# Kernel optimization log

Hardware: AMD Instinct MI355X
Metric: run time of the kernel (lower is better)

Reference implementation:

```python
import jax, jax.numpy as jnp
import numpy as np

Q_MAX = 127.0  # 2^(8-1) - 1 for 8-bit activations


def _ste_round(x):
    # forward: round(x); backward: identity
    return x + jax.lax.stop_gradient(jnp.round(x) - x)


def setup_inputs() -> dict:
    key = jax.random.key(0)
    k1, k2 = jax.random.split(key)
    B, S, D_IN, D_OUT = 4, 4096, 2048, 2048
    x = jax.random.normal(k1, (B, S, D_IN), dtype=jnp.float32)
    # muP-style init: std = 1/sqrt(fan_in)
    weight = jax.random.normal(k2, (D_OUT, D_IN), dtype=jnp.float32) / np.sqrt(D_IN)
    return {"x": x, "weight": weight}


def reference(x, weight):
    # --- ternary weight quantization (AbsMean) ---
    w_scale = jnp.maximum(jnp.mean(jnp.abs(weight)), 1e-6)        # scalar
    w_norm = weight / w_scale
    w_quant = jnp.clip(_ste_round(w_norm), -1.0, 1.0)             # [O, I], values in {-1,0,1}

    # --- per-token absmax activation quantization (8-bit) ---
    a_scale = jnp.clip(jnp.max(jnp.abs(x), axis=-1, keepdims=True), 1e-8, None)  # [B,S,1]
    x_quant = jnp.clip(_ste_round(x * (Q_MAX / a_scale)), -Q_MAX, Q_MAX)         # [B,S,I]

    # --- scaled matmul: y = (x_q @ w_q^T) * w_scale * (a_scale / Q_MAX) ---
    y = jnp.einsum('bsi,oi->bso', x_quant, w_quant)
    y = y * (w_scale * (a_scale / Q_MAX))
    return y
```

## Files before the change

### kernel.cpp

```cpp
#include <hip/hip_runtime.h>
#include <hip/hip_bf16.h>

typedef int int4v __attribute__((ext_vector_type(4)));

#define K_DIM 2048
#define N_DIM 2048
#define M_DIM 16384
#define NW 4194304
#define BKB 128
#define NKT (K_DIM / BKB)

__global__ void k_wsum(const float4* __restrict__ w4, double* __restrict__ red) {
  const int n4 = NW / 4;
  double s = 0.0;
  for (int i = blockIdx.x * blockDim.x + threadIdx.x; i < n4; i += gridDim.x * blockDim.x) {
    float4 v = w4[i];
    s += (double)fabsf(v.x) + (double)fabsf(v.y) + (double)fabsf(v.z) + (double)fabsf(v.w);
  }
  for (int o = 32; o; o >>= 1) s += __shfl_xor(s, o);
  __shared__ double sd[4];
  if ((threadIdx.x & 63) == 0) sd[threadIdx.x >> 6] = s;
  __syncthreads();
  if (threadIdx.x == 0) red[blockIdx.x] = (sd[0] + sd[1]) + (sd[2] + sd[3]);
}

__global__ void k_wscale(const double* __restrict__ red, double* __restrict__ wsd) {
  double s = red[threadIdx.x];
  for (int o = 32; o; o >>= 1) s += __shfl_xor(s, o);
  __shared__ double sd[4];
  if ((threadIdx.x & 63) == 0) sd[threadIdx.x >> 6] = s;
  __syncthreads();
  if (threadIdx.x == 0) {
    double m = ((sd[0] + sd[1]) + (sd[2] + sd[3])) / (double)NW;
    *wsd = (m > 1e-6) ? m : 1e-6;
  }
}

__device__ __forceinline__ char wq1(float v, double ws) {
  double r = rint((double)v / ws);
  r = fmin(fmax(r, -1.0), 1.0);
  return (char)(int)r;
}

__global__ void k_wquant(const float4* __restrict__ w4, const double* __restrict__ wsd,
                         char4* __restrict__ wq4) {
  int i = blockIdx.x * blockDim.x + threadIdx.x;
  if (i >= NW / 4) return;
  double ws = *wsd;
  float4 v = w4[i];
  char4 q;
  q.x = wq1(v.x, ws);
  q.y = wq1(v.y, ws);
  q.z = wq1(v.z, ws);
  q.w = wq1(v.w, ws);
  wq4[i] = q;
}

__device__ __forceinline__ char qi8(float v, double rr) {
  double q = rint((double)v * rr);
  q = fmin(fmax(q, -127.0), 127.0);
  return (char)(int)q;
}

__global__ void k_xquant(const float* __restrict__ x, float* __restrict__ ascale,
                         char* __restrict__ xq) {
  const int row = blockIdx.x;
  const int t = threadIdx.x;
  const float4* xr = (const float4*)(x + (size_t)row * K_DIM);
  float4 v0 = xr[t];
  float4 v1 = xr[t + 256];
  float m = fmaxf(fmaxf(fmaxf(fabsf(v0.x), fabsf(v0.y)), fmaxf(fabsf(v0.z), fabsf(v0.w))),
                  fmaxf(fmaxf(fabsf(v1.x), fabsf(v1.y)), fmaxf(fabsf(v1.z), fabsf(v1.w))));
  for (int o = 32; o; o >>= 1) m = fmaxf(m, __shfl_xor(m, o));
  __shared__ float sm[4];
  if ((t & 63) == 0) sm[t >> 6] = m;
  __syncthreads();
  float a = fmaxf(fmaxf(sm[0], sm[1]), fmaxf(sm[2], sm[3]));
  a = fmaxf(a, 1e-8f);
  if (t == 0) ascale[row] = a;
  double rr = 127.0 / (double)a;
  char4* qr4 = (char4*)(xq + (size_t)row * K_DIM);
  char4 a4, b4;
  a4.x = qi8(v0.x, rr); a4.y = qi8(v0.y, rr); a4.z = qi8(v0.z, rr); a4.w = qi8(v0.w, rr);
  b4.x = qi8(v1.x, rr); b4.y = qi8(v1.y, rr); b4.z = qi8(v1.z, rr); b4.w = qi8(v1.w, rr);
  qr4[t] = a4;
  qr4[t + 256] = b4;
}

__device__ __forceinline__ void gload16(const void* g, void* l) {
  __builtin_amdgcn_global_load_lds(
      (const __attribute__((address_space(1))) void*)g,
      (__attribute__((address_space(3))) void*)l, 16, 0, 0);
}

#define RD_A(DST, CA, MH, CO)                                               \
  _Pragma("unroll") for (int mf = 0; mf < 4; ++mf)                          \
    DST[mf] = *(const int4v*)((CA) + (rA + (MH)*64 + mf * 16) * 128 + (CO));

#define MM(MH, AF, BF)                                                      \
  __builtin_amdgcn_s_setprio(1);                                            \
  _Pragma("unroll") for (int mf = 0; mf < 4; ++mf)                          \
  _Pragma("unroll") for (int nf = 0; nf < 4; ++nf)                          \
    acc[(MH)*4 + mf][nf] = __builtin_amdgcn_mfma_i32_16x16x64_i8(           \
        AF[mf], BF[nf], acc[(MH)*4 + mf][nf], 0, 0, 0);                     \
  __builtin_amdgcn_s_setprio(0);

__global__ __launch_bounds__(512, 1) void k_gemm(
    const char* __restrict__ xq, const char* __restrict__ wq,
    const float* __restrict__ ascale, const double* __restrict__ wsd,
    float* __restrict__ out) {
  __shared__ __align__(16) char lds[98304];

  const int tid = threadIdx.x;
  const int l = tid & 63;
  const int wv = tid >> 6;
  const int wm = wv >> 2;
  const int wn = wv & 3;
  const int g = l >> 4, r16 = l & 15;

  const int bid = blockIdx.x;
  const int logical = (bid & 7) * 64 + (bid >> 3);
  const int br = logical >> 3;
  const int bc = logical & 7;

  const char* Ab = xq + (size_t)br * 256 * K_DIM;
  const char* Bb = wq + (size_t)bc * 256 * K_DIM;

  int soff[4], loff[4];
#pragma unroll
  for (int c = 0; c < 4; ++c) {
    int lb = c * 8192 + tid * 16;
    loff[c] = lb;
    int row = lb >> 7;
    int cb = lb & 127;
    soff[c] = row * K_DIM + (cb ^ ((row & 7) << 4));
  }

  const int sw = (r16 & 7) << 4;
  const int co0 = (g * 16) ^ sw;
  const int co1 = (64 + g * 16) ^ sw;
  const int rA = wm * 128 + r16;

  int sB[4];
#pragma unroll
  for (int nf = 0; nf < 4; ++nf)
    sB[nf] = (wn * 64 + nf * 16 + r16) * K_DIM + g * 16;

  int4v acc[8][4];
#pragma unroll
  for (int mf = 0; mf < 8; ++mf)
#pragma unroll
    for (int nf = 0; nf < 4; ++nf) acc[mf][nf] = (int4v){0, 0, 0, 0};

#pragma unroll
  for (int c = 0; c < 4; ++c) gload16(Ab + soff[c], lds + loff[c]);

  int4v af0[4], af1[4], af2[4];
  int4v bq0[4], bq1[4];

  for (int kt = 0; kt < NKT; ++kt) {
    char* cbuf = lds + (kt % 3) * 32768;
    char* nbuf = lds + ((kt + 1) % 3) * 32768;
    const char* An = Ab + (((kt + 1) & (NKT - 1)) * BKB);
    const int ko = kt * BKB;

#pragma unroll
    for (int c = 0; c < 4; ++c) gload16(An + soff[c], nbuf + loff[c]);
#pragma unroll
    for (int nf = 0; nf < 4; ++nf) {
      bq0[nf] = *(const int4v*)(Bb + sB[nf] + ko);
      bq1[nf] = *(const int4v*)(Bb + sB[nf] + ko + 64);
    }

    asm volatile("s_waitcnt vmcnt(12)" ::: "memory");
    __builtin_amdgcn_s_barrier();

    RD_A(af0, cbuf, 0, co0);
    RD_A(af1, cbuf, 1, co0);
    RD_A(af2, cbuf, 0, co1);
    MM(0, af0, bq0);
    MM(1, af1, bq0);
    RD_A(af0, cbuf, 1, co1);
    MM(0, af2, bq1);
    MM(1, af0, bq1);
  }

  float wsf = (float)(*wsd);
  size_t trow0 = (size_t)br * 256 + wm * 128;
  int oc0 = bc * 256 + wn * 64;
#pragma unroll
  for (int mf = 0; mf < 8; ++mf) {
#pragma unroll
    for (int j = 0; j < 4; ++j) {
      size_t t = trow0 + mf * 16 + g * 4 + j;
      float s = wsf * (ascale[t] / 127.0f);
      float* yr = out + t * (size_t)N_DIM + oc0;
#pragma unroll
      for (int nf = 0; nf < 4; ++nf) yr[nf * 16 + r16] = (float)acc[mf][nf][j] * s;
    }
  }
}

extern "C" void kernel_launch(void* const* d_in, const int* in_sizes, int n_in,
                              void* d_out, int out_size, void* d_ws, size_t ws_size,
                              hipStream_t stream) {
  const float* x = (const float*)d_in[0];
  const float* w = (const float*)d_in[1];
  float* out = (float*)d_out;

  char* ws = (char*)d_ws;
  double* red = (double*)ws;
  double* wsd = (double*)(ws + 2048);
  float* ascale = (float*)(ws + 4096);
  char* xq = (char*)(ws + 4096 + 65536);
  char* wq = xq + (size_t)M_DIM * K_DIM;

  k_wsum<<<256, 256, 0, stream>>>((const float4*)w, red);
  k_wscale<<<1, 256, 0, stream>>>(red, wsd);
  k_wquant<<<NW / 4 / 256, 256, 0, stream>>>((const float4*)w, wsd, (char4*)wq);
  k_xquant<<<M_DIM, 256, 0, stream>>>(x, ascale, xq);
  k_gemm<<<dim3(N_DIM / 256 * M_DIM / 256), 512, 0, stream>>>(xq, wq, ascale, wsd, out);
}
```

Measured before the change: 143.0 us.

## Restructure int8 GEMM with 32x32 MFMA, LDS-staged B, and fused weight-scale reduction

The GEMM moves from 512 threads using 16x16x64 MFMA, with B read straight from global memory, to 256 threads using 32x32x32 MFMA. Each wave now computes a 128x128 subtile, and both A and B are staged through a double-buffered swizzled LDS layout. Loads for the next K tile are issued while the current tile's MFMAs run, with a full vmcnt(0) wait and barrier per tile. The separate single-block weight-scale kernel is folded into the weight-quant kernel, where every block redundantly re-reduces the partial sums, saving one launch. The changes aim to cut global B traffic and raise MFMA efficiency, at the cost of fewer waves per CU and a stricter wait per tile.

```diff
diff --git a/kernel.cpp b/kernel.cpp
--- a/kernel.cpp
+++ b/kernel.cpp
@@ -2,6 +2,7 @@
 #include <hip/hip_bf16.h>
 
 typedef int int4v __attribute__((ext_vector_type(4)));
+typedef int int16v __attribute__((ext_vector_type(16)));
 
 #define K_DIM 2048
 #define N_DIM 2048
@@ -24,29 +25,24 @@
   if (threadIdx.x == 0) red[blockIdx.x] = (sd[0] + sd[1]) + (sd[2] + sd[3]);
 }
 
-__global__ void k_wscale(const double* __restrict__ red, double* __restrict__ wsd) {
-  double s = red[threadIdx.x];
-  for (int o = 32; o; o >>= 1) s += __shfl_xor(s, o);
-  __shared__ double sd[4];
-  if ((threadIdx.x & 63) == 0) sd[threadIdx.x >> 6] = s;
-  __syncthreads();
-  if (threadIdx.x == 0) {
-    double m = ((sd[0] + sd[1]) + (sd[2] + sd[3])) / (double)NW;
-    *wsd = (m > 1e-6) ? m : 1e-6;
-  }
-}
-
 __device__ __forceinline__ char wq1(float v, double ws) {
   double r = rint((double)v / ws);
   r = fmin(fmax(r, -1.0), 1.0);
   return (char)(int)r;
 }
 
-__global__ void k_wquant(const float4* __restrict__ w4, const double* __restrict__ wsd,
-                         char4* __restrict__ wq4) {
+__global__ void k_wquant(const float4* __restrict__ w4, const double* __restrict__ red,
+                         double* __restrict__ wsd, char4* __restrict__ wq4) {
+  __shared__ double sd[4];
+  double s = red[threadIdx.x];
+  for (int o = 32; o; o >>= 1) s += __shfl_xor(s, o);
+  if ((threadIdx.x & 63) == 0) sd[threadIdx.x >> 6] = s;
+  __syncthreads();
+  double m = ((sd[0] + sd[1]) + (sd[2] + sd[3])) / (double)NW;
+  double ws = (m > 1e-6) ? m : 1e-6;
+  if (blockIdx.x == 0 && threadIdx.x == 0) *wsd = ws;
   int i = blockIdx.x * blockDim.x + threadIdx.x;
   if (i >= NW / 4) return;
-  double ws = *wsd;
   float4 v = w4[i];
   char4 q;
   q.x = wq1(v.x, ws);
@@ -93,30 +89,61 @@
       (__attribute__((address_space(3))) void*)l, 16, 0, 0);
 }
 
-#define RD_A(DST, CA, MH, CO)                                               \
+#define RD_A(DST, CA, KS)                                                   \
   _Pragma("unroll") for (int mf = 0; mf < 4; ++mf)                          \
-    DST[mf] = *(const int4v*)((CA) + (rA + (MH)*64 + mf * 16) * 128 + (CO));
-
-#define MM(MH, AF, BF)                                                      \
-  __builtin_amdgcn_s_setprio(1);                                            \
+    DST[mf] = *(const int4v*)((CA) + (rA + mf * 32) * 128 + co[KS]);
+
+#define RD_B(DST, CB, KS)                                                   \
+  _Pragma("unroll") for (int nf = 0; nf < 4; ++nf)                          \
+    DST[nf] = *(const int4v*)((CB) + (rB + nf * 32) * 128 + co[KS]);
+
+#define MM(AF, BF)                                                          \
   _Pragma("unroll") for (int mf = 0; mf < 4; ++mf)                          \
   _Pragma("unroll") for (int nf = 0; nf < 4; ++nf)                          \
-    acc[(MH)*4 + mf][nf] = __builtin_amdgcn_mfma_i32_16x16x64_i8(           \
-        AF[mf], BF[nf], acc[(MH)*4 + mf][nf], 0, 0, 0);                     \
-  __builtin_amdgcn_s_setprio(0);
-
-__global__ __launch_bounds__(512, 1) void k_gemm(
+    acc[mf][nf] = __builtin_amdgcn_mfma_i32_32x32x32_i8(                    \
+        AF[mf], BF[nf], acc[mf][nf], 0, 0, 0);
+
+#define TILE(CA, CB, NA, NB, KT)                                            \
+  {                                                                         \
+    const char* An = Ab + (((KT) + 1) & (NKT - 1)) * BKB;                   \
+    const char* Bn = Bb + (((KT) + 1) & (NKT - 1)) * BKB;                   \
+    RD_A(aX, CA, 0);                                                        \
+    RD_B(bX, CB, 0);                                                        \
+    _Pragma("unroll") for (int c = 0; c < 8; ++c)                           \
+      gload16(An + soff[c], (NA) + loff[c]);                                \
+    RD_A(aY, CA, 1);                                                        \
+    RD_B(bY, CB, 1);                                                        \
+    _Pragma("unroll") for (int c = 0; c < 8; ++c)                           \
+      gload16(Bn + soff[c], (NB) + loff[c]);                                \
+    MM(aX, bX);                                                             \
+    RD_A(aX, CA, 2);                                                        \
+    RD_B(bX, CB, 2);                                                        \
+    MM(aY, bY);                                                             \
+    RD_A(aY, CA, 3);                                                        \
+    RD_B(bY, CB, 3);                                                        \
+    MM(aX, bX);                                                             \
+    MM(aY, bY);                                                             \
+    asm volatile("s_waitcnt vmcnt(0)" ::: "memory");                        \
+    __builtin_amdgcn_s_barrier();                                           \
+  }
+
+__global__ __launch_bounds__(256, 1) void k_gemm(
     const char* __restrict__ xq, const char* __restrict__ wq,
     const float* __restrict__ ascale, const double* __restrict__ wsd,
     float* __restrict__ out) {
-  __shared__ __align__(16) char lds[98304];
+  __shared__ __align__(16) char lds[131072];
+  char* A0 = lds;
+  char* B0 = lds + 32768;
+  char* A1 = lds + 65536;
+  char* B1 = lds + 98304;
 
   const int tid = threadIdx.x;
   const int l = tid & 63;
   const int wv = tid >> 6;
-  const int wm = wv >> 2;
-  const int wn = wv & 3;
-  const int g = l >> 4, r16 = l & 15;
+  const int wm = wv >> 1;
+  const int wn = wv & 1;
+  const int r32 = l & 31;
+  const int hk = (l >> 5) * 16;
 
   const int bid = blockIdx.x;
   const int logical = (bid & 7) * 64 + (bid >> 3);
@@ -126,77 +153,58 @@
   const char* Ab = xq + (size_t)br * 256 * K_DIM;
   const char* Bb = wq + (size_t)bc * 256 * K_DIM;
 
-  int soff[4], loff[4];
-#pragma unroll
-  for (int c = 0; c < 4; ++c) {
-    int lb = c * 8192 + tid * 16;
+  int soff[8], loff[8];
+#pragma unroll
+  for (int c = 0; c < 8; ++c) {
+    int lb = c * 4096 + tid * 16;
     loff[c] = lb;
     int row = lb >> 7;
     int cb = lb & 127;
     soff[c] = row * K_DIM + (cb ^ ((row & 7) << 4));
   }
 
-  const int sw = (r16 & 7) << 4;
-  const int co0 = (g * 16) ^ sw;
-  const int co1 = (64 + g * 16) ^ sw;
-  const int rA = wm * 128 + r16;
-
-  int sB[4];
-#pragma unroll
-  for (int nf = 0; nf < 4; ++nf)
-    sB[nf] = (wn * 64 + nf * 16 + r16) * K_DIM + g * 16;
-
-  int4v acc[8][4];
-#pragma unroll
-  for (int mf = 0; mf < 8; ++mf)
-#pragma unroll
-    for (int nf = 0; nf < 4; ++nf) acc[mf][nf] = (int4v){0, 0, 0, 0};
-
-#pragma unroll
-  for (int c = 0; c < 4; ++c) gload16(Ab + soff[c], lds + loff[c]);
-
-  int4v af0[4], af1[4], af2[4];
-  int4v bq0[4], bq1[4];
-
-  for (int kt = 0; kt < NKT; ++kt) {
-    char* cbuf = lds + (kt % 3) * 32768;
-    char* nbuf = lds + ((kt + 1) % 3) * 32768;
-    const char* An = Ab + (((kt + 1) & (NKT - 1)) * BKB);
-    const int ko = kt * BKB;
-
-#pragma unroll
-    for (int c = 0; c < 4; ++c) gload16(An + soff[c], nbuf + loff[c]);
-#pragma unroll
-    for (int nf = 0; nf < 4; ++nf) {
-      bq0[nf] = *(const int4v*)(Bb + sB[nf] + ko);
-      bq1[nf] = *(const int4v*)(Bb + sB[nf] + ko + 64);
-    }
-
-    asm volatile("s_waitcnt vmcnt(12)" ::: "memory");
-    __builtin_amdgcn_s_barrier();
-
-    RD_A(af0, cbuf, 0, co0);
-    RD_A(af1, cbuf, 1, co0);
-    RD_A(af2, cbuf, 0, co1);
-    MM(0, af0, bq0);
-    MM(1, af1, bq0);
-    RD_A(af0, cbuf, 1, co1);
-    MM(0, af2, bq1);
-    MM(1, af0, bq1);
+  const int sw = (l & 7) << 4;
+  int co[4];
+#pragma unroll
+  for (int k = 0; k < 4; ++k) co[k] = (k * 32 + hk) ^ sw;
+  const int rA = wm * 128 + r32;
+  const int rB = wn * 128 + r32;
+
+  int16v acc[4][4];
+#pragma unroll
+  for (int mf = 0; mf < 4; ++mf)
+#pragma unroll
+    for (int nf = 0; nf < 4; ++nf)
+#pragma unroll
+      for (int j = 0; j < 16; ++j) acc[mf][nf][j] = 0;
+
+#pragma unroll
+  for (int c = 0; c < 8; ++c) gload16(Ab + soff[c], A0 + loff[c]);
+#pragma unroll
+  for (int c = 0; c < 8; ++c) gload16(Bb + soff[c], B0 + loff[c]);
+  asm volatile("s_waitcnt vmcnt(0)" ::: "memory");
+  __builtin_amdgcn_s_barrier();
+
+  int4v aX[4], aY[4], bX[4], bY[4];
+
+  for (int kt = 0; kt < NKT; kt += 2) {
+    TILE(A0, B0, A1, B1, kt);
+    TILE(A1, B1, A0, B0, kt + 1);
   }
 
   float wsf = (float)(*wsd);
-  size_t trow0 = (size_t)br * 256 + wm * 128;
-  int oc0 = bc * 256 + wn * 64;
-#pragma unroll
-  for (int mf = 0; mf < 8; ++mf) {
-#pragma unroll
-    for (int j = 0; j < 4; ++j) {
-      size_t t = trow0 + mf * 16 + g * 4 + j;
-      float s = wsf * (ascale[t] / 127.0f);
-      float* yr = out + t * (size_t)N_DIM + oc0;
-#pragma unroll
-      for (int nf = 0; nf < 4; ++nf) yr[nf * 16 + r16] = (float)acc[mf][nf][j] * s;
+  size_t r0 = (size_t)br * 256 + wm * 128;
+  int c0 = bc * 256 + wn * 128;
+#pragma unroll
+  for (int mf = 0; mf < 4; ++mf) {
+#pragma unroll
+    for (int j = 0; j < 16; ++j) {
+      size_t row = r0 + mf * 32 + (j & 3) + 8 * (j >> 2) + 4 * (l >> 5);
+      float s = wsf * (ascale[row] / 127.0f);
+      float* yr = out + row * (size_t)N_DIM + c0;
+#pragma unroll
+      for (int nf = 0; nf < 4; ++nf)
+        yr[nf * 32 + r32] = (float)acc[mf][nf][j] * s;
     }
   }
 }
@@ -216,8 +224,7 @@
   char* wq = xq + (size_t)M_DIM * K_DIM;
 
   k_wsum<<<256, 256, 0, stream>>>((const float4*)w, red);
-  k_wscale<<<1, 256, 0, stream>>>(red, wsd);
-  k_wquant<<<NW / 4 / 256, 256, 0, stream>>>((const float4*)w, wsd, (char4*)wq);
+  k_wquant<<<NW / 4 / 256, 256, 0, stream>>>((const float4*)w, red, wsd, (char4*)wq);
   k_xquant<<<M_DIM, 256, 0, stream>>>(x, ascale, xq);
-  k_gemm<<<dim3(N_DIM / 256 * M_DIM / 256), 512, 0, stream>>>(xq, wq, ascale, wsd, out);
-}
+  k_gemm<<<dim3(N_DIM / 256 * M_DIM / 256), 256, 0, stream>>>(xq, wq, ascale, wsd, out);
+}
```

Result: slower. 183.5 us (+28.3%).

## Stage both GEMM operands through a 4-buffer LDS pipeline and fuse weight-scale kernels

Applied to the files above, without the earlier changes.

The GEMM now loads both the activation and weight tiles into LDS with direct global-to-LDS loads. It uses BK=64 tiles in a four-slot ring that prefetches two tiles ahead, with a swizzled layout. Before, the weight fragments were read straight from global memory into registers on every iteration. On the host side, the abs-sum reduction of the weights is folded into the activation-quantize kernel and the final scale reduction into the weight-quantize kernel, removing two launches. The cost is twice the LDS footprint and more barriers per K step, and every wquant block now redundantly recomputes the scale reduction.

```diff
diff --git a/kernel.cpp b/kernel.cpp
--- a/kernel.cpp
+++ b/kernel.cpp
@@ -7,54 +7,8 @@
 #define N_DIM 2048
 #define M_DIM 16384
 #define NW 4194304
-#define BKB 128
-#define NKT (K_DIM / BKB)
-
-__global__ void k_wsum(const float4* __restrict__ w4, double* __restrict__ red) {
-  const int n4 = NW / 4;
-  double s = 0.0;
-  for (int i = blockIdx.x * blockDim.x + threadIdx.x; i < n4; i += gridDim.x * blockDim.x) {
-    float4 v = w4[i];
-    s += (double)fabsf(v.x) + (double)fabsf(v.y) + (double)fabsf(v.z) + (double)fabsf(v.w);
-  }
-  for (int o = 32; o; o >>= 1) s += __shfl_xor(s, o);
-  __shared__ double sd[4];
-  if ((threadIdx.x & 63) == 0) sd[threadIdx.x >> 6] = s;
-  __syncthreads();
-  if (threadIdx.x == 0) red[blockIdx.x] = (sd[0] + sd[1]) + (sd[2] + sd[3]);
-}
-
-__global__ void k_wscale(const double* __restrict__ red, double* __restrict__ wsd) {
-  double s = red[threadIdx.x];
-  for (int o = 32; o; o >>= 1) s += __shfl_xor(s, o);
-  __shared__ double sd[4];
-  if ((threadIdx.x & 63) == 0) sd[threadIdx.x >> 6] = s;
-  __syncthreads();
-  if (threadIdx.x == 0) {
-    double m = ((sd[0] + sd[1]) + (sd[2] + sd[3])) / (double)NW;
-    *wsd = (m > 1e-6) ? m : 1e-6;
-  }
-}
-
-__device__ __forceinline__ char wq1(float v, double ws) {
-  double r = rint((double)v / ws);
-  r = fmin(fmax(r, -1.0), 1.0);
-  return (char)(int)r;
-}
-
-__global__ void k_wquant(const float4* __restrict__ w4, const double* __restrict__ wsd,
-                         char4* __restrict__ wq4) {
-  int i = blockIdx.x * blockDim.x + threadIdx.x;
-  if (i >= NW / 4) return;
-  double ws = *wsd;
-  float4 v = w4[i];
-  char4 q;
-  q.x = wq1(v.x, ws);
-  q.y = wq1(v.y, ws);
-  q.z = wq1(v.z, ws);
-  q.w = wq1(v.w, ws);
-  wq4[i] = q;
-}
+#define BKB 64
+#define NKT 32
 
 __device__ __forceinline__ char qi8(float v, double rr) {
   double q = rint((double)v * rr);
@@ -63,7 +17,8 @@
 }
 
 __global__ void k_xquant(const float* __restrict__ x, float* __restrict__ ascale,
-                         char* __restrict__ xq) {
+                         char* __restrict__ xq, const float4* __restrict__ w4,
+                         double* __restrict__ red) {
   const int row = blockIdx.x;
   const int t = threadIdx.x;
   const float4* xr = (const float4*)(x + (size_t)row * K_DIM);
@@ -85,6 +40,47 @@
   b4.x = qi8(v1.x, rr); b4.y = qi8(v1.y, rr); b4.z = qi8(v1.z, rr); b4.w = qi8(v1.w, rr);
   qr4[t] = a4;
   qr4[t + 256] = b4;
+
+  if (row < 256) {
+    const int n4 = NW / 4;
+    double s = 0.0;
+    for (int i = row * 256 + t; i < n4; i += 256 * 256) {
+      float4 v = w4[i];
+      s += (double)fabsf(v.x) + (double)fabsf(v.y) + (double)fabsf(v.z) + (double)fabsf(v.w);
+    }
+    for (int o = 32; o; o >>= 1) s += __shfl_xor(s, o);
+    __shared__ double sd[4];
+    if ((t & 63) == 0) sd[t >> 6] = s;
+    __syncthreads();
+    if (t == 0) red[row] = (sd[0] + sd[1]) + (sd[2] + sd[3]);
+  }
+}
+
+__device__ __forceinline__ char wq1(float v, double ws) {
+  double r = rint((double)v / ws);
+  r = fmin(fmax(r, -1.0), 1.0);
+  return (char)(int)r;
+}
+
+__global__ void k_wquant(const float4* __restrict__ w4, const double* __restrict__ red,
+                         double* __restrict__ wsd, char4* __restrict__ wq4) {
+  __shared__ double sd[4];
+  double s = red[threadIdx.x];
+  for (int o = 32; o; o >>= 1) s += __shfl_xor(s, o);
+  if ((threadIdx.x & 63) == 0) sd[threadIdx.x >> 6] = s;
+  __syncthreads();
+  double m = ((sd[0] + sd[1]) + (sd[2] + sd[3])) / (double)NW;
+  double ws = (m > 1e-6) ? m : 1e-6;
+  if (blockIdx.x == 0 && threadIdx.x == 0) *wsd = ws;
+  int i = blockIdx.x * blockDim.x + threadIdx.x;
+  if (i >= NW / 4) return;
+  float4 v = w4[i];
+  char4 q;
+  q.x = wq1(v.x, ws);
+  q.y = wq1(v.y, ws);
+  q.z = wq1(v.z, ws);
+  q.w = wq1(v.w, ws);
+  wq4[i] = q;
 }
 
 __device__ __forceinline__ void gload16(const void* g, void* l) {
@@ -93,9 +89,13 @@
       (__attribute__((address_space(3))) void*)l, 16, 0, 0);
 }
 
-#define RD_A(DST, CA, MH, CO)                                               \
+#define RD_A(DST, CA, MH)                                                   \
   _Pragma("unroll") for (int mf = 0; mf < 4; ++mf)                          \
-    DST[mf] = *(const int4v*)((CA) + (rA + (MH)*64 + mf * 16) * 128 + (CO));
+    DST[mf] = *(const int4v*)((CA) + (rA + (MH)*64 + mf * 16) * 64 + co);
+
+#define RD_B(DST, CB)                                                       \
+  _Pragma("unroll") for (int nf = 0; nf < 4; ++nf)                          \
+    DST[nf] = *(const int4v*)((CB) + (rB + nf * 16) * 64 + co);
 
 #define MM(MH, AF, BF)                                                      \
   __builtin_amdgcn_s_setprio(1);                                            \
@@ -105,11 +105,36 @@
         AF[mf], BF[nf], acc[(MH)*4 + mf][nf], 0, 0, 0);                     \
   __builtin_amdgcn_s_setprio(0);
 
+#define SBAR __builtin_amdgcn_s_barrier()
+#define VM4  asm volatile("s_waitcnt vmcnt(4)" ::: "memory")
+
+#define TILE64(CI, SI, KT)                                                  \
+  {                                                                         \
+    const char* cb_ = lds + (CI)*32768;                                     \
+    char* sb_ = lds + (SI)*32768;                                           \
+    const int kk = ((KT) + 2) & (NKT - 1);                                  \
+                          \
+    RD_B(bf, cb_ + 16384);                                                  \
+    RD_A(af, cb_, 0);                                                       \
+    SBAR;                                                                   \
+    gload16(Ab + kk * BKB + soff[0], sb_ + loff[0]);                        \
+    gload16(Ab + kk * BKB + soff[1], sb_ + loff[1]);                        \
+    MM(0, af, bf);                                                          \
+               \
+    RD_A(af2, cb_, 1);                                                      \
+    SBAR;                                                                   \
+    gload16(Bb + kk * BKB + soff[0], sb_ + 16384 + loff[0]);                \
+    gload16(Bb + kk * BKB + soff[1], sb_ + 16384 + loff[1]);                \
+    MM(1, af2, bf);                                                         \
+    VM4;                                                                    \
+    SBAR;                                                                   \
+  }
+
 __global__ __launch_bounds__(512, 1) void k_gemm(
     const char* __restrict__ xq, const char* __restrict__ wq,
     const float* __restrict__ ascale, const double* __restrict__ wsd,
     float* __restrict__ out) {
-  __shared__ __align__(16) char lds[98304];
+  __shared__ __align__(16) char lds[131072];
 
   const int tid = threadIdx.x;
   const int l = tid & 63;
@@ -126,25 +151,19 @@
   const char* Ab = xq + (size_t)br * 256 * K_DIM;
   const char* Bb = wq + (size_t)bc * 256 * K_DIM;
 
-  int soff[4], loff[4];
-#pragma unroll
-  for (int c = 0; c < 4; ++c) {
+  int soff[2], loff[2];
+#pragma unroll
+  for (int c = 0; c < 2; ++c) {
     int lb = c * 8192 + tid * 16;
     loff[c] = lb;
-    int row = lb >> 7;
-    int cb = lb & 127;
-    soff[c] = row * K_DIM + (cb ^ ((row & 7) << 4));
-  }
-
-  const int sw = (r16 & 7) << 4;
-  const int co0 = (g * 16) ^ sw;
-  const int co1 = (64 + g * 16) ^ sw;
+    int row = lb >> 6;
+    int cb = lb & 63;
+    soff[c] = row * K_DIM + (cb ^ ((row & 3) << 4));
+  }
+
+  const int co = (g * 16) ^ ((r16 & 3) << 4);
   const int rA = wm * 128 + r16;
-
-  int sB[4];
-#pragma unroll
-  for (int nf = 0; nf < 4; ++nf)
-    sB[nf] = (wn * 64 + nf * 16 + r16) * K_DIM + g * 16;
+  const int rB = wn * 64 + r16;
 
   int4v acc[8][4];
 #pragma unroll
@@ -153,36 +172,25 @@
     for (int nf = 0; nf < 4; ++nf) acc[mf][nf] = (int4v){0, 0, 0, 0};
 
 #pragma unroll
-  for (int c = 0; c < 4; ++c) gload16(Ab + soff[c], lds + loff[c]);
-
-  int4v af0[4], af1[4], af2[4];
-  int4v bq0[4], bq1[4];
-
-  for (int kt = 0; kt < NKT; ++kt) {
-    char* cbuf = lds + (kt % 3) * 32768;
-    char* nbuf = lds + ((kt + 1) % 3) * 32768;
-    const char* An = Ab + (((kt + 1) & (NKT - 1)) * BKB);
-    const int ko = kt * BKB;
-
-#pragma unroll
-    for (int c = 0; c < 4; ++c) gload16(An + soff[c], nbuf + loff[c]);
-#pragma unroll
-    for (int nf = 0; nf < 4; ++nf) {
-      bq0[nf] = *(const int4v*)(Bb + sB[nf] + ko);
-      bq1[nf] = *(const int4v*)(Bb + sB[nf] + ko + 64);
-    }
-
-    asm volatile("s_waitcnt vmcnt(12)" ::: "memory");
-    __builtin_amdgcn_s_barrier();
-
-    RD_A(af0, cbuf, 0, co0);
-    RD_A(af1, cbuf, 1, co0);
-    RD_A(af2, cbuf, 0, co1);
-    MM(0, af0, bq0);
-    MM(1, af1, bq0);
-    RD_A(af0, cbuf, 1, co1);
-    MM(0, af2, bq1);
-    MM(1, af0, bq1);
+  for (int c = 0; c < 2; ++c) {
+    gload16(Ab + soff[c], lds + loff[c]);
+    gload16(Bb + soff[c], lds + 16384 + loff[c]);
+  }
+#pragma unroll
+  for (int c = 0; c < 2; ++c) {
+    gload16(Ab + BKB + soff[c], lds + 32768 + loff[c]);
+    gload16(Bb + BKB + soff[c], lds + 32768 + 16384 + loff[c]);
+  }
+  VM4;
+  SBAR;
+
+  int4v af[4], af2[4], bf[4];
+
+  for (int kt = 0; kt < NKT; kt += 4) {
+    TILE64(0, 2, kt);
+    TILE64(1, 3, kt + 1);
+    TILE64(2, 0, kt + 2);
+    TILE64(3, 1, kt + 3);
   }
 
   float wsf = (float)(*wsd);
@@ -215,9 +223,7 @@
   char* xq = (char*)(ws + 4096 + 65536);
   char* wq = xq + (size_t)M_DIM * K_DIM;
 
-  k_wsum<<<256, 256, 0, stream>>>((const float4*)w, red);
-  k_wscale<<<1, 256, 0, stream>>>(red, wsd);
-  k_wquant<<<NW / 4 / 256, 256, 0, stream>>>((const float4*)w, wsd, (char4*)wq);
-  k_xquant<<<M_DIM, 256, 0, stream>>>(x, ascale, xq);
+  k_xquant<<<M_DIM, 256, 0, stream>>>(x, ascale, xq, (const float4*)w, red);
+  k_wquant<<<NW / 4 / 256, 256, 0, stream>>>((const float4*)w, red, wsd, (char4*)wq);
   k_gemm<<<dim3(N_DIM / 256 * M_DIM / 256), 512, 0, stream>>>(xq, wq, ascale, wsd, out);
 }
```

New measurement: 122.5 us. 14.4% less time.
